# Kernel tuning notes

Measured on AMD Instinct MI355X. Metric: run time of the kernel, lower is better.

The kernel has to match this reference:

```python
import jax, jax.numpy as jnp
import numpy as np

EPS = 1e-5  # torch BatchNorm2d default


def _conv1x1(x, w):
    # x: [n, cin, h, w], w: [cout, cin] (1x1 conv == per-pixel matmul)
    return jnp.einsum('nchw,oc->nohw', x, w)


def _bn(x, gamma, beta, mean, var):
    # inference-mode BatchNorm2d over channel dim
    scale = gamma * jax.lax.rsqrt(var + EPS)
    shift = beta - mean * scale
    return x * scale[None, :, None, None] + shift[None, :, None, None]


def setup_inputs() -> dict:
    key = jax.random.key(0)
    ks = jax.random.split(key, 24)
    n, c, h, w = 16, 256, 64, 64
    width, planes = c // 2, c
    inp = {
        'x': jax.random.normal(ks[0], (n, c, h, w), jnp.float32),
        'w_theta': jax.random.normal(ks[1], (width, c), jnp.float32) * 0.05,
        'w_phi': jax.random.normal(ks[2], (width, c), jnp.float32) * 0.05,
        'w_g': jax.random.normal(ks[3], (width, c), jnp.float32) * 0.05,
        'w_zeta': jax.random.normal(ks[4], (planes, width), jnp.float32) * 0.05,
    }
    for i, (name, dim) in enumerate([('bn1', width), ('bn2', width), ('bn3', width), ('bn4', planes)]):
        k = 5 + 4 * i
        inp[f'{name}_gamma'] = jax.random.uniform(ks[k], (dim,), jnp.float32, 0.5, 1.5)
        inp[f'{name}_beta'] = jax.random.normal(ks[k + 1], (dim,), jnp.float32) * 0.1
        inp[f'{name}_mean'] = jax.random.normal(ks[k + 2], (dim,), jnp.float32) * 0.1
        inp[f'{name}_var'] = jax.random.uniform(ks[k + 3], (dim,), jnp.float32, 0.5, 1.5)
    return inp


def reference(x, w_theta, w_phi, w_g, w_zeta,
              bn1_gamma, bn1_beta, bn1_mean, bn1_var,
              bn2_gamma, bn2_beta, bn2_mean, bn2_var,
              bn3_gamma, bn3_beta, bn3_mean, bn3_var,
              bn4_gamma, bn4_beta, bn4_mean, bn4_var):
    n, c, h, w = x.shape
    theta = jax.nn.relu(_bn(_conv1x1(x, w_theta), bn1_gamma, bn1_beta, bn1_mean, bn1_var))
    phi = jax.nn.relu(_bn(_conv1x1(x, w_phi), bn2_gamma, bn2_beta, bn2_mean, bn2_var))
    g = jax.nn.relu(_bn(_conv1x1(x, w_g), bn3_gamma, bn3_beta, bn3_mean, bn3_var))

    width = theta.shape[1]
    hw = h * w
    theta = theta.reshape(n, width, hw)  # [n, C', S]
    phi = phi.reshape(n, width, hw)      # [n, C', S]
    g = g.reshape(n, width, hw)          # [n, C', S]

    # (theta^T @ phi) @ g^T == theta^T @ (phi @ g^T): no softmax, so associativity
    # lets us contract over pixels first -> O(S*C'^2) instead of O(S^2*C').
    kv = jnp.einsum('ncs,nds->ncd', phi, g)      # [n, C', C']
    out = jnp.einsum('ncs,ncd->nsd', theta, kv)  # [n, S, C']

    # faithful to torch: reshape (not transpose) [n, S, C'] -> [n, C', h, w]
    out = out.reshape(n, width, h, w)
    out = _bn(_conv1x1(out, w_zeta), bn4_gamma, bn4_beta, bn4_mean, bn4_var)
    return jax.nn.relu(out + x)
```

## Files before the change

kernel.cpp:

```cpp
#include <hip/hip_runtime.h>

#define BN_EPS 1e-5f

typedef unsigned short u16;
typedef __bf16 bf16x8 __attribute__((ext_vector_type(8)));
typedef float floatx4 __attribute__((ext_vector_type(4)));
typedef u16 u16x4 __attribute__((ext_vector_type(4)));
typedef u16 u16x8 __attribute__((ext_vector_type(8)));

__device__ __forceinline__ u16 f2bf(float f) {
    union { float f; unsigned int u; } v; v.f = f;
    unsigned int r = (v.u + 0x7fffu + ((v.u >> 16) & 1u)) >> 16;
    return (u16)r;
}

__device__ __forceinline__ unsigned int cvtpk(float lo, float hi) {
    unsigned int r;
    asm("v_cvt_pk_bf16_f32 %0, %1, %2" : "=v"(r) : "v"(lo), "v"(hi));
    return r;
}

__device__ __forceinline__ void gld16(const void* gsrc, void* ldst) {
    __builtin_amdgcn_global_load_lds(
        (const __attribute__((address_space(1))) unsigned int*)gsrc,
        (__attribute__((address_space(3))) unsigned int*)ldst, 16, 0, 0);
}

__device__ __forceinline__ int addsw(int seg, int s) {
    return (seg + (s & 7) + ((s >> 3) & 7)) & 7;
}

__global__ __launch_bounds__(256) void prep_kernel(
    const float* __restrict__ wt, const float* __restrict__ wp,
    const float* __restrict__ wg, const float* __restrict__ wz,
    const float* __restrict__ g1, const float* __restrict__ b1,
    const float* __restrict__ m1, const float* __restrict__ v1,
    const float* __restrict__ g2, const float* __restrict__ b2,
    const float* __restrict__ m2, const float* __restrict__ v2,
    const float* __restrict__ g3, const float* __restrict__ b3,
    const float* __restrict__ m3, const float* __restrict__ v3,
    const float* __restrict__ g4, const float* __restrict__ b4,
    const float* __restrict__ m4, const float* __restrict__ v4,
    u16* __restrict__ W1bf, float* __restrict__ shift1,
    u16* __restrict__ Wzbf, float* __restrict__ shift4)
{
    int id = blockIdx.x * 256 + threadIdx.x;
    if (id < 384 * 256) {
        int r = id >> 8, c = id & 255;
        int grp = r >> 7, ch = r & 127;
        const float* wsrc = grp == 0 ? wt : (grp == 1 ? wp : wg);
        const float* gg = grp == 0 ? g1 : (grp == 1 ? g2 : g3);
        const float* bb = grp == 0 ? b1 : (grp == 1 ? b2 : b3);
        const float* mm = grp == 0 ? m1 : (grp == 1 ? m2 : m3);
        const float* vv = grp == 0 ? v1 : (grp == 1 ? v2 : v3);
        float scale = gg[ch] * rsqrtf(vv[ch] + BN_EPS);
        W1bf[id] = f2bf(wsrc[ch * 256 + c] * scale);
        if (c == 0) shift1[r] = bb[ch] - mm[ch] * scale;
    }
    if (id < 256 * 128) {
        int o = id >> 7;
        float scale = g4[o] * rsqrtf(v4[o] + BN_EPS);
        Wzbf[id] = f2bf(wz[id] * scale);
        if ((id & 127) == 0) shift4[o] = b4[o] - m4[o] * scale;
    }
}

__global__ __launch_bounds__(512, 4) void gemm1_kernel(
    const float* __restrict__ x, const u16* __restrict__ W1,
    const float* __restrict__ shift1,
    u16* __restrict__ theta_sm, u16* __restrict__ pg)
{
    const int st = blockIdx.x, n = blockIdx.y;
    const int tid = threadIdx.x;
    const int w = tid >> 6, lane = tid & 63;
    const int quad = lane >> 4, l16 = lane & 15;

    __shared__ __align__(16) u16 ldsA[384 * 64];
    __shared__ __align__(16) u16 ldsB[64 * 64];

    floatx4 acc[3][4];
#pragma unroll
    for (int i = 0; i < 3; ++i)
#pragma unroll
        for (int j = 0; j < 4; ++j) acc[i][j] = floatx4{0.f, 0.f, 0.f, 0.f};

    const int s4 = tid & 15;
    const int cg = tid >> 4;
    const int slog = cg >> 2, dwin = cg & 3;
    const float* xb0 = x + ((size_t)n * 256 + 2 * cg) * 4096 + st * 64;
    unsigned int* ldsBdw = (unsigned int*)ldsB;

    float4 xv0 = *((const float4*)xb0 + s4);
    float4 xv1 = *((const float4*)(xb0 + 4096) + s4);

    for (int kc = 0; kc < 4; ++kc) {
        const float* f0 = (const float*)&xv0;
        const float* f1 = (const float*)&xv1;
#pragma unroll
        for (int j = 0; j < 4; ++j) {
            int s = 4 * s4 + j;
            ldsBdw[s * 32 + addsw(slog, s) * 4 + dwin] = cvtpk(f0[j], f1[j]);
        }
#pragma unroll
        for (int i = 0; i < 6; ++i) {
            int op = w * 6 + i;
            int r = op * 8 + (lane >> 3);
            int lseg = (lane & 7) ^ (r & 7);
            gld16(W1 + (size_t)r * 256 + kc * 64 + lseg * 8, ldsA + op * 512);
        }
        if (kc < 3) {
            xv0 = *((const float4*)(xb0 + (size_t)(kc + 1) * 64 * 4096) + s4);
            xv1 = *((const float4*)(xb0 + (size_t)((kc + 1) * 64 + 1) * 4096) + s4);
        }
        __syncthreads();

#pragma unroll
        for (int kk = 0; kk < 2; ++kk) {
            bf16x8 a[3];
#pragma unroll
            for (int mt = 0; mt < 3; ++mt) {
                int r = mt * 128 + w * 16 + l16;
                int phys = (kk * 4 + quad) ^ (r & 7);
                a[mt] = *(const bf16x8*)(ldsA + r * 64 + phys * 8);
            }
#pragma unroll
            for (int ni = 0; ni < 4; ++ni) {
                int s = ni * 16 + l16;
                int phys = addsw(kk * 4 + quad, s);
                bf16x8 b = *(const bf16x8*)(ldsB + s * 64 + phys * 8);
#pragma unroll
                for (int mt = 0; mt < 3; ++mt)
                    acc[mt][ni] = __builtin_amdgcn_mfma_f32_16x16x32_bf16(
                        a[mt], b, acc[mt][ni], 0, 0, 0);
            }
        }
        __syncthreads();
    }

    const int ocq = w * 16 + quad * 4;

    {
        float sh0 = shift1[ocq + 0], sh1 = shift1[ocq + 1];
        float sh2 = shift1[ocq + 2], sh3 = shift1[ocq + 3];
#pragma unroll
        for (int ni = 0; ni < 4; ++ni) {
            int s = st * 64 + ni * 16 + l16;
            float v0 = acc[0][ni][0] + sh0, v1 = acc[0][ni][1] + sh1;
            float v2 = acc[0][ni][2] + sh2, v3 = acc[0][ni][3] + sh3;
            v0 = v0 > 0.f ? v0 : 0.f;
            v1 = v1 > 0.f ? v1 : 0.f;
            v2 = v2 > 0.f ? v2 : 0.f;
            v3 = v3 > 0.f ? v3 : 0.f;
            uint2 pk;
            pk.x = cvtpk(v0, v1);
            pk.y = cvtpk(v2, v3);
            *(uint2*)(theta_sm + (size_t)n * 524288 + (size_t)s * 128 + ocq) = pk;
        }
    }

#pragma unroll
    for (int mt = 1; mt < 3; ++mt)
#pragma unroll
        for (int r = 0; r < 4; ++r) {
            int oc = mt * 128 + ocq + r;
            int prow = oc - 128;
            float sh = shift1[oc];
#pragma unroll
            for (int ni = 0; ni < 4; ++ni) {
                int s = st * 64 + ni * 16 + l16;
                float val = acc[mt][ni][r] + sh;
                val = val > 0.f ? val : 0.f;
                pg[(size_t)n * 1048576 + (size_t)prow * 4096 + s] = f2bf(val);
            }
        }
}

__global__ __launch_bounds__(512) void gemm2_kernel(
    const u16* __restrict__ pg, float* __restrict__ partials)
{
    const int kc = blockIdx.x, n = blockIdx.y;
    const int tid = threadIdx.x;
    const int w = tid >> 6, lane = tid & 63;
    const int quad = lane >> 4, l16 = lane & 15;

    __shared__ __align__(16) u16 ldsG[128 * 64];
    __shared__ __align__(16) u16 ldsP[128 * 64];

    floatx4 acc[2][4];
#pragma unroll
    for (int i = 0; i < 2; ++i)
#pragma unroll
        for (int j = 0; j < 4; ++j) acc[i][j] = floatx4{0.f, 0.f, 0.f, 0.f};

    const int d0 = (w >> 1) * 32, c0 = (w & 1) * 64;
    const u16* base = pg + (size_t)n * 1048576;

    for (int ch = 0; ch < 4; ++ch) {
        int s0 = kc * 256 + ch * 64;
#pragma unroll
        for (int i = 0; i < 2; ++i) {
            int op = w * 2 + i;
            int r = op * 8 + (lane >> 3);
            int lseg = (lane & 7) ^ (r & 7);
            gld16(base + (size_t)(128 + r) * 4096 + s0 + lseg * 8, ldsG + op * 512);
            gld16(base + (size_t)r * 4096 + s0 + lseg * 8, ldsP + op * 512);
        }
        __syncthreads();

#pragma unroll
        for (int kk = 0; kk < 2; ++kk) {
            bf16x8 a[2];
#pragma unroll
            for (int mi = 0; mi < 2; ++mi) {
                int r = d0 + mi * 16 + l16;
                int phys = (kk * 4 + quad) ^ (r & 7);
                a[mi] = *(const bf16x8*)(ldsG + r * 64 + phys * 8);
            }
#pragma unroll
            for (int ci = 0; ci < 4; ++ci) {
                int r = c0 + ci * 16 + l16;
                int phys = (kk * 4 + quad) ^ (r & 7);
                bf16x8 b = *(const bf16x8*)(ldsP + r * 64 + phys * 8);
#pragma unroll
                for (int mi = 0; mi < 2; ++mi)
                    acc[mi][ci] = __builtin_amdgcn_mfma_f32_16x16x32_bf16(
                        a[mi], b, acc[mi][ci], 0, 0, 0);
            }
        }
        __syncthreads();
    }

    float* outp = partials + (size_t)(n * 16 + kc) * 16384;
#pragma unroll
    for (int mi = 0; mi < 2; ++mi)
#pragma unroll
        for (int r = 0; r < 4; ++r) {
            int d = d0 + mi * 16 + quad * 4 + r;
#pragma unroll
            for (int ci = 0; ci < 4; ++ci)
                outp[d * 128 + c0 + ci * 16 + l16] = acc[mi][ci][r];
        }
}

__global__ __launch_bounds__(256) void kv_reduce_kernel(
    const float* __restrict__ partials, u16* __restrict__ kvT)
{
    int n = blockIdx.y;
    int f4 = blockIdx.x * 256 + threadIdx.x;
    const float4* p4 = (const float4*)partials;
    float4 s = {0.f, 0.f, 0.f, 0.f};
#pragma unroll
    for (int kc = 0; kc < 16; ++kc) {
        float4 v = p4[(size_t)(n * 16 + kc) * 4096 + f4];
        s.x += v.x; s.y += v.y; s.z += v.z; s.w += v.w;
    }
    u16x4 o; o[0] = f2bf(s.x); o[1] = f2bf(s.y); o[2] = f2bf(s.z); o[3] = f2bf(s.w);
    *(u16x4*)(kvT + (size_t)n * 16384 + f4 * 4) = o;
}

__global__ __launch_bounds__(256) void gemm3_kernel(
    const u16* __restrict__ theta_sm, const u16* __restrict__ kvT,
    u16* __restrict__ out_sd)
{
    const int st = blockIdx.x, n = blockIdx.y;
    const int tid = threadIdx.x;
    const int w = tid >> 6, lane = tid & 63;
    const int quad = lane >> 4, l16 = lane & 15;

    __shared__ __align__(16) u16 ldsT[128 * 64];
    __shared__ __align__(16) u16 ldsK[128 * 64];

    floatx4 acc[2][8];
#pragma unroll
    for (int i = 0; i < 2; ++i)
#pragma unroll
        for (int j = 0; j < 8; ++j) acc[i][j] = floatx4{0.f, 0.f, 0.f, 0.f};

    const u16* tbase = theta_sm + (size_t)n * 524288 + (size_t)st * 128 * 128;
    const u16* kbase = kvT + (size_t)n * 16384;

    for (int ch = 0; ch < 2; ++ch) {
#pragma unroll
        for (int i = 0; i < 4; ++i) {
            int op = w * 4 + i;
            int r = op * 8 + (lane >> 3);
            int lseg = (lane & 7) ^ (r & 7);
            gld16(tbase + (size_t)r * 128 + ch * 64 + lseg * 8, ldsT + op * 512);
            gld16(kbase + (size_t)r * 128 + ch * 64 + lseg * 8, ldsK + op * 512);
        }
        __syncthreads();

#pragma unroll
        for (int kk = 0; kk < 2; ++kk) {
            bf16x8 a[2];
#pragma unroll
            for (int mi = 0; mi < 2; ++mi) {
                int r = w * 32 + mi * 16 + l16;
                int phys = (kk * 4 + quad) ^ (r & 7);
                a[mi] = *(const bf16x8*)(ldsT + r * 64 + phys * 8);
            }
#pragma unroll
            for (int di = 0; di < 8; ++di) {
                int r = di * 16 + l16;
                int phys = (kk * 4 + quad) ^ (r & 7);
                bf16x8 b = *(const bf16x8*)(ldsK + r * 64 + phys * 8);
#pragma unroll
                for (int mi = 0; mi < 2; ++mi)
                    acc[mi][di] = __builtin_amdgcn_mfma_f32_16x16x32_bf16(
                        a[mi], b, acc[mi][di], 0, 0, 0);
            }
        }
        __syncthreads();
    }

#pragma unroll
    for (int mi = 0; mi < 2; ++mi)
#pragma unroll
        for (int r = 0; r < 4; ++r) {
            int s = st * 128 + w * 32 + mi * 16 + quad * 4 + r;
#pragma unroll
            for (int di = 0; di < 8; ++di)
                out_sd[(size_t)n * 524288 + (size_t)s * 128 + di * 16 + l16] =
                    f2bf(acc[mi][di][r]);
        }
}

__global__ __launch_bounds__(256) void gemm4_kernel(
    const u16* __restrict__ out_sd, const u16* __restrict__ Wz,
    const float* __restrict__ shift4, const float* __restrict__ x,
    float* __restrict__ out)
{
    const int st = blockIdx.x, ot = blockIdx.y, n = blockIdx.z;
    const int tid = threadIdx.x;
    const int w = tid >> 6, lane = tid & 63;
    const int quad = lane >> 4, l16 = lane & 15;

    __shared__ __align__(16) u16 ldsY[128 * 64];
    __shared__ __align__(16) u16 ldsW[128 * 64];

    floatx4 acc[2][8];
#pragma unroll
    for (int i = 0; i < 2; ++i)
#pragma unroll
        for (int j = 0; j < 8; ++j) acc[i][j] = floatx4{0.f, 0.f, 0.f, 0.f};

    const int sl = tid & 15;
    const int cg = tid >> 4;
    const u16* ybase = out_sd + (size_t)n * 524288 + st * 128;
    unsigned int* ldsYdw = (unsigned int*)ldsY;

    u16x8 yv0[2], yv1[2];
#pragma unroll
    for (int p = 0; p < 2; ++p) {
        int c0 = 2 * cg + 32 * p;
        yv0[p] = *(const u16x8*)(ybase + (size_t)c0 * 4096 + 8 * sl);
        yv1[p] = *(const u16x8*)(ybase + (size_t)(c0 + 1) * 4096 + 8 * sl);
    }

    for (int kc = 0; kc < 2; ++kc) {
#pragma unroll
        for (int p = 0; p < 2; ++p) {
            int cp = cg + 16 * p, slog = cp >> 2, dwin = cp & 3;
#pragma unroll
            for (int j = 0; j < 8; ++j) {
                int s = 8 * sl + j;
                unsigned int pk = (unsigned int)yv0[p][j] | ((unsigned int)yv1[p][j] << 16);
                ldsYdw[s * 32 + addsw(slog, s) * 4 + dwin] = pk;
            }
        }
#pragma unroll
        for (int i = 0; i < 4; ++i) {
            int op = w * 4 + i;
            int r = op * 8 + (lane >> 3);
            int lseg = (lane & 7) ^ (r & 7);
            gld16(Wz + (size_t)(ot * 128 + r) * 128 + kc * 64 + lseg * 8, ldsW + op * 512);
        }
        if (kc < 1) {
#pragma unroll
            for (int p = 0; p < 2; ++p) {
                int c0 = 2 * cg + 32 * p;
                yv0[p] = *(const u16x8*)(ybase + (size_t)(64 + c0) * 4096 + 8 * sl);
                yv1[p] = *(const u16x8*)(ybase + (size_t)(64 + c0 + 1) * 4096 + 8 * sl);
            }
        }
        __syncthreads();

#pragma unroll
        for (int kk = 0; kk < 2; ++kk) {
            bf16x8 a[2];
#pragma unroll
            for (int mi = 0; mi < 2; ++mi) {
                int r = w * 32 + mi * 16 + l16;
                int phys = (kk * 4 + quad) ^ (r & 7);
                a[mi] = *(const bf16x8*)(ldsW + r * 64 + phys * 8);
            }
#pragma unroll
            for (int ni = 0; ni < 8; ++ni) {
                int s = ni * 16 + l16;
                int phys = addsw(kk * 4 + quad, s);
                bf16x8 b = *(const bf16x8*)(ldsY + s * 64 + phys * 8);
#pragma unroll
                for (int mi = 0; mi < 2; ++mi)
                    acc[mi][ni] = __builtin_amdgcn_mfma_f32_16x16x32_bf16(
                        a[mi], b, acc[mi][ni], 0, 0, 0);
            }
        }
        __syncthreads();
    }

#pragma unroll
    for (int mi = 0; mi < 2; ++mi)
#pragma unroll
        for (int r = 0; r < 4; ++r) {
            int o = ot * 128 + w * 32 + mi * 16 + quad * 4 + r;
            float sh = shift4[o];
#pragma unroll
            for (int ni = 0; ni < 8; ++ni) {
                int s2 = st * 128 + ni * 16 + l16;
                size_t idx = ((size_t)n * 256 + o) * 4096 + s2;
                float val = acc[mi][ni][r] + sh + x[idx];
                out[idx] = val > 0.f ? val : 0.f;
            }
        }
}

extern "C" void kernel_launch(void* const* d_in, const int* in_sizes, int n_in,
                              void* d_out, int out_size, void* d_ws, size_t ws_size,
                              hipStream_t stream)
{
    const float* x  = (const float*)d_in[0];
    const float* wt = (const float*)d_in[1];
    const float* wp = (const float*)d_in[2];
    const float* wg = (const float*)d_in[3];
    const float* wz = (const float*)d_in[4];
    const float* bn[16];
    for (int i = 0; i < 16; ++i) bn[i] = (const float*)d_in[5 + i];

    char* ws = (char*)d_ws;
    u16*   W1bf     = (u16*)  (ws + 0);
    float* shift1   = (float*)(ws + 196608);
    u16*   Wzbf     = (u16*)  (ws + 198144);
    float* shift4   = (float*)(ws + 263680);
    u16*   theta_sm = (u16*)  (ws + 264704);
    u16*   pg       = (u16*)  (ws + 17041920);
    float* partials = (float*)(ws + 50596352);
    u16*   kvT      = (u16*)  (ws + 67373568);
    u16*   out_sd   = (u16*)  (ws + 67897856);
    float* out = (float*)d_out;

    prep_kernel<<<384, 256, 0, stream>>>(
        wt, wp, wg, wz,
        bn[0], bn[1], bn[2], bn[3],
        bn[4], bn[5], bn[6], bn[7],
        bn[8], bn[9], bn[10], bn[11],
        bn[12], bn[13], bn[14], bn[15],
        W1bf, shift1, Wzbf, shift4);

    gemm1_kernel<<<dim3(64, 16), 512, 0, stream>>>(x, W1bf, shift1, theta_sm, pg);
    gemm2_kernel<<<dim3(16, 16), 512, 0, stream>>>(pg, partials);
    kv_reduce_kernel<<<dim3(16, 16), 256, 0, stream>>>(partials, kvT);
    gemm3_kernel<<<dim3(32, 16), 256, 0, stream>>>(theta_sm, kvT, out_sd);
    gemm4_kernel<<<dim3(32, 2, 16), 256, 0, stream>>>(out_sd, Wzbf, shift4, x, out);
}
```

Baseline: 220.2 us.

## Double-buffer LDS in all GEMM kernels and widen gemm1 pixel tile

```diff
diff --git a/kernel.cpp b/kernel.cpp
--- a/kernel.cpp
+++ b/kernel.cpp
@@ -65,7 +65,7 @@
     }
 }
 
-__global__ __launch_bounds__(512, 4) void gemm1_kernel(
+__global__ __launch_bounds__(512, 2) void gemm1_kernel(
     const float* __restrict__ x, const u16* __restrict__ W1,
     const float* __restrict__ shift1,
     u16* __restrict__ theta_sm, u16* __restrict__ pg)
@@ -75,45 +75,48 @@
     const int w = tid >> 6, lane = tid & 63;
     const int quad = lane >> 4, l16 = lane & 15;
 
-    __shared__ __align__(16) u16 ldsA[384 * 64];
-    __shared__ __align__(16) u16 ldsB[64 * 64];
-
-    floatx4 acc[3][4];
+    __shared__ __align__(16) u16 ldsA[2][384 * 64];
+    __shared__ __align__(16) u16 ldsB[2][128 * 64];
+
+    floatx4 acc[3][8];
 #pragma unroll
     for (int i = 0; i < 3; ++i)
 #pragma unroll
-        for (int j = 0; j < 4; ++j) acc[i][j] = floatx4{0.f, 0.f, 0.f, 0.f};
-
-    const int s4 = tid & 15;
-    const int cg = tid >> 4;
-    const int slog = cg >> 2, dwin = cg & 3;
-    const float* xb0 = x + ((size_t)n * 256 + 2 * cg) * 4096 + st * 64;
-    unsigned int* ldsBdw = (unsigned int*)ldsB;
-
-    float4 xv0 = *((const float4*)xb0 + s4);
-    float4 xv1 = *((const float4*)(xb0 + 4096) + s4);
-
-    for (int kc = 0; kc < 4; ++kc) {
-        const float* f0 = (const float*)&xv0;
-        const float* f1 = (const float*)&xv1;
-#pragma unroll
-        for (int j = 0; j < 4; ++j) {
-            int s = 4 * s4 + j;
-            ldsBdw[s * 32 + addsw(slog, s) * 4 + dwin] = cvtpk(f0[j], f1[j]);
-        }
+        for (int j = 0; j < 8; ++j) acc[i][j] = floatx4{0.f, 0.f, 0.f, 0.f};
+
+    const int cp = w * 4 + quad;
+    const float* xb = x + ((size_t)n * 256 + 2 * cp) * 4096 + st * 128;
+
+    float4 xva[2][2], xvb[2][2];
+
+    auto loadx = [&](float4 (&xv)[2][2], int kc) {
+#pragma unroll
+        for (int ch = 0; ch < 2; ++ch)
+#pragma unroll
+            for (int hb = 0; hb < 2; ++hb)
+                xv[ch][hb] = *((const float4*)(xb + (size_t)(kc * 64 + ch) * 4096) + hb * 16 + l16);
+    };
+    auto writeB = [&](int buf, const float4 (&xv)[2][2]) {
+        unsigned int* bd = (unsigned int*)ldsB[buf];
+#pragma unroll
+        for (int hb = 0; hb < 2; ++hb)
+#pragma unroll
+            for (int j = 0; j < 4; ++j) {
+                int s = hb * 64 + l16 * 4 + j;
+                bd[s * 32 + addsw(w, s) * 4 + quad] =
+                    cvtpk(((const float*)&xv[0][hb])[j], ((const float*)&xv[1][hb])[j]);
+            }
+    };
+    auto stageA = [&](int buf, int kc) {
 #pragma unroll
         for (int i = 0; i < 6; ++i) {
             int op = w * 6 + i;
             int r = op * 8 + (lane >> 3);
             int lseg = (lane & 7) ^ (r & 7);
-            gld16(W1 + (size_t)r * 256 + kc * 64 + lseg * 8, ldsA + op * 512);
-        }
-        if (kc < 3) {
-            xv0 = *((const float4*)(xb0 + (size_t)(kc + 1) * 64 * 4096) + s4);
-            xv1 = *((const float4*)(xb0 + (size_t)((kc + 1) * 64 + 1) * 4096) + s4);
-        }
-        __syncthreads();
-
+            gld16(W1 + (size_t)r * 256 + kc * 64 + lseg * 8, ldsA[buf] + op * 512);
+        }
+    };
+    auto compute = [&](int buf) {
 #pragma unroll
         for (int kk = 0; kk < 2; ++kk) {
             bf16x8 a[3];
@@ -121,30 +124,50 @@
             for (int mt = 0; mt < 3; ++mt) {
                 int r = mt * 128 + w * 16 + l16;
                 int phys = (kk * 4 + quad) ^ (r & 7);
-                a[mt] = *(const bf16x8*)(ldsA + r * 64 + phys * 8);
-            }
-#pragma unroll
-            for (int ni = 0; ni < 4; ++ni) {
+                a[mt] = *(const bf16x8*)(ldsA[buf] + r * 64 + phys * 8);
+            }
+#pragma unroll
+            for (int ni = 0; ni < 8; ++ni) {
                 int s = ni * 16 + l16;
                 int phys = addsw(kk * 4 + quad, s);
-                bf16x8 b = *(const bf16x8*)(ldsB + s * 64 + phys * 8);
+                bf16x8 b = *(const bf16x8*)(ldsB[buf] + s * 64 + phys * 8);
 #pragma unroll
                 for (int mt = 0; mt < 3; ++mt)
                     acc[mt][ni] = __builtin_amdgcn_mfma_f32_16x16x32_bf16(
                         a[mt], b, acc[mt][ni], 0, 0, 0);
             }
         }
-        __syncthreads();
-    }
+    };
+
+    loadx(xva, 0);
+    stageA(0, 0);
+    writeB(0, xva);
+    loadx(xvb, 1);
+    __syncthreads();
+
+    loadx(xva, 2);
+    stageA(1, 1);
+    writeB(1, xvb);
+    compute(0);
+    __syncthreads();
+    loadx(xvb, 3);
+    stageA(0, 2);
+    writeB(0, xva);
+    compute(1);
+    __syncthreads();
+    stageA(1, 3);
+    writeB(1, xvb);
+    compute(0);
+    __syncthreads();
+    compute(1);
 
     const int ocq = w * 16 + quad * 4;
-
     {
         float sh0 = shift1[ocq + 0], sh1 = shift1[ocq + 1];
         float sh2 = shift1[ocq + 2], sh3 = shift1[ocq + 3];
 #pragma unroll
-        for (int ni = 0; ni < 4; ++ni) {
-            int s = st * 64 + ni * 16 + l16;
+        for (int ni = 0; ni < 8; ++ni) {
+            int s = st * 128 + ni * 16 + l16;
             float v0 = acc[0][ni][0] + sh0, v1 = acc[0][ni][1] + sh1;
             float v2 = acc[0][ni][2] + sh2, v3 = acc[0][ni][3] + sh3;
             v0 = v0 > 0.f ? v0 : 0.f;
@@ -157,7 +180,6 @@
             *(uint2*)(theta_sm + (size_t)n * 524288 + (size_t)s * 128 + ocq) = pk;
         }
     }
-
 #pragma unroll
     for (int mt = 1; mt < 3; ++mt)
 #pragma unroll
@@ -166,8 +188,8 @@
             int prow = oc - 128;
             float sh = shift1[oc];
 #pragma unroll
-            for (int ni = 0; ni < 4; ++ni) {
-                int s = st * 64 + ni * 16 + l16;
+            for (int ni = 0; ni < 8; ++ni) {
+                int s = st * 128 + ni * 16 + l16;
                 float val = acc[mt][ni][r] + sh;
                 val = val > 0.f ? val : 0.f;
                 pg[(size_t)n * 1048576 + (size_t)prow * 4096 + s] = f2bf(val);
@@ -183,8 +205,8 @@
     const int w = tid >> 6, lane = tid & 63;
     const int quad = lane >> 4, l16 = lane & 15;
 
-    __shared__ __align__(16) u16 ldsG[128 * 64];
-    __shared__ __align__(16) u16 ldsP[128 * 64];
+    __shared__ __align__(16) u16 ldsG[2][128 * 64];
+    __shared__ __align__(16) u16 ldsP[2][128 * 64];
 
     floatx4 acc[2][4];
 #pragma unroll
@@ -195,18 +217,18 @@
     const int d0 = (w >> 1) * 32, c0 = (w & 1) * 64;
     const u16* base = pg + (size_t)n * 1048576;
 
-    for (int ch = 0; ch < 4; ++ch) {
+    auto stage = [&](int buf, int ch) {
         int s0 = kc * 256 + ch * 64;
 #pragma unroll
         for (int i = 0; i < 2; ++i) {
             int op = w * 2 + i;
             int r = op * 8 + (lane >> 3);
             int lseg = (lane & 7) ^ (r & 7);
-            gld16(base + (size_t)(128 + r) * 4096 + s0 + lseg * 8, ldsG + op * 512);
-            gld16(base + (size_t)r * 4096 + s0 + lseg * 8, ldsP + op * 512);
-        }
-        __syncthreads();
-
+            gld16(base + (size_t)(128 + r) * 4096 + s0 + lseg * 8, ldsG[buf] + op * 512);
+            gld16(base + (size_t)r * 4096 + s0 + lseg * 8, ldsP[buf] + op * 512);
+        }
+    };
+    auto comp = [&](int buf) {
 #pragma unroll
         for (int kk = 0; kk < 2; ++kk) {
             bf16x8 a[2];
@@ -214,21 +236,26 @@
             for (int mi = 0; mi < 2; ++mi) {
                 int r = d0 + mi * 16 + l16;
                 int phys = (kk * 4 + quad) ^ (r & 7);
-                a[mi] = *(const bf16x8*)(ldsG + r * 64 + phys * 8);
+                a[mi] = *(const bf16x8*)(ldsG[buf] + r * 64 + phys * 8);
             }
 #pragma unroll
             for (int ci = 0; ci < 4; ++ci) {
                 int r = c0 + ci * 16 + l16;
                 int phys = (kk * 4 + quad) ^ (r & 7);
-                bf16x8 b = *(const bf16x8*)(ldsP + r * 64 + phys * 8);
+                bf16x8 b = *(const bf16x8*)(ldsP[buf] + r * 64 + phys * 8);
 #pragma unroll
                 for (int mi = 0; mi < 2; ++mi)
                     acc[mi][ci] = __builtin_amdgcn_mfma_f32_16x16x32_bf16(
                         a[mi], b, acc[mi][ci], 0, 0, 0);
             }
         }
-        __syncthreads();
-    }
+    };
+
+    stage(0, 0); __syncthreads();
+    stage(1, 1); comp(0); __syncthreads();
+    stage(0, 2); comp(1); __syncthreads();
+    stage(1, 3); comp(0); __syncthreads();
+    comp(1);
 
     float* outp = partials + (size_t)(n * 16 + kc) * 16384;
 #pragma unroll
@@ -267,8 +294,8 @@
     const int w = tid >> 6, lane = tid & 63;
     const int quad = lane >> 4, l16 = lane & 15;
 
-    __shared__ __align__(16) u16 ldsT[128 * 64];
-    __shared__ __align__(16) u16 ldsK[128 * 64];
+    __shared__ __align__(16) u16 ldsT[2][128 * 64];
+    __shared__ __align__(16) u16 ldsK[2][128 * 64];
 
     floatx4 acc[2][8];
 #pragma unroll
@@ -279,17 +306,17 @@
     const u16* tbase = theta_sm + (size_t)n * 524288 + (size_t)st * 128 * 128;
     const u16* kbase = kvT + (size_t)n * 16384;
 
-    for (int ch = 0; ch < 2; ++ch) {
+    auto stage = [&](int buf, int ch) {
 #pragma unroll
         for (int i = 0; i < 4; ++i) {
             int op = w * 4 + i;
             int r = op * 8 + (lane >> 3);
             int lseg = (lane & 7) ^ (r & 7);
-            gld16(tbase + (size_t)r * 128 + ch * 64 + lseg * 8, ldsT + op * 512);
-            gld16(kbase + (size_t)r * 128 + ch * 64 + lseg * 8, ldsK + op * 512);
-        }
-        __syncthreads();
-
+            gld16(tbase + (size_t)r * 128 + ch * 64 + lseg * 8, ldsT[buf] + op * 512);
+            gld16(kbase + (size_t)r * 128 + ch * 64 + lseg * 8, ldsK[buf] + op * 512);
+        }
+    };
+    auto comp = [&](int buf) {
 #pragma unroll
         for (int kk = 0; kk < 2; ++kk) {
             bf16x8 a[2];
@@ -297,21 +324,24 @@
             for (int mi = 0; mi < 2; ++mi) {
                 int r = w * 32 + mi * 16 + l16;
                 int phys = (kk * 4 + quad) ^ (r & 7);
-                a[mi] = *(const bf16x8*)(ldsT + r * 64 + phys * 8);
+                a[mi] = *(const bf16x8*)(ldsT[buf] + r * 64 + phys * 8);
             }
 #pragma unroll
             for (int di = 0; di < 8; ++di) {
                 int r = di * 16 + l16;
                 int phys = (kk * 4 + quad) ^ (r & 7);
-                bf16x8 b = *(const bf16x8*)(ldsK + r * 64 + phys * 8);
+                bf16x8 b = *(const bf16x8*)(ldsK[buf] + r * 64 + phys * 8);
 #pragma unroll
                 for (int mi = 0; mi < 2; ++mi)
                     acc[mi][di] = __builtin_amdgcn_mfma_f32_16x16x32_bf16(
                         a[mi], b, acc[mi][di], 0, 0, 0);
             }
         }
-        __syncthreads();
-    }
+    };
+
+    stage(0, 0); __syncthreads();
+    stage(1, 1); comp(0); __syncthreads();
+    comp(1);
 
 #pragma unroll
     for (int mi = 0; mi < 2; ++mi)
@@ -335,8 +365,8 @@
     const int w = tid >> 6, lane = tid & 63;
     const int quad = lane >> 4, l16 = lane & 15;
 
-    __shared__ __align__(16) u16 ldsY[128 * 64];
-    __shared__ __align__(16) u16 ldsW[128 * 64];
+    __shared__ __align__(16) u16 ldsY[2][128 * 64];
+    __shared__ __align__(16) u16 ldsW[2][128 * 64];
 
     floatx4 acc[2][8];
 #pragma unroll
@@ -347,44 +377,41 @@
     const int sl = tid & 15;
     const int cg = tid >> 4;
     const u16* ybase = out_sd + (size_t)n * 524288 + st * 128;
-    unsigned int* ldsYdw = (unsigned int*)ldsY;
-
-    u16x8 yv0[2], yv1[2];
-#pragma unroll
-    for (int p = 0; p < 2; ++p) {
-        int c0 = 2 * cg + 32 * p;
-        yv0[p] = *(const u16x8*)(ybase + (size_t)c0 * 4096 + 8 * sl);
-        yv1[p] = *(const u16x8*)(ybase + (size_t)(c0 + 1) * 4096 + 8 * sl);
-    }
-
-    for (int kc = 0; kc < 2; ++kc) {
+    unsigned int* ldsYdw0 = (unsigned int*)ldsY[0];
+    unsigned int* ldsYdw1 = (unsigned int*)ldsY[1];
+
+    u16x8 ya0[2], ya1[2], yb0[2], yb1[2];
+
+    auto loadY = [&](u16x8 (&y0)[2], u16x8 (&y1)[2], int kc) {
+#pragma unroll
+        for (int p = 0; p < 2; ++p) {
+            int c0 = 2 * cg + 32 * p + kc * 64;
+            y0[p] = *(const u16x8*)(ybase + (size_t)c0 * 4096 + 8 * sl);
+            y1[p] = *(const u16x8*)(ybase + (size_t)(c0 + 1) * 4096 + 8 * sl);
+        }
+    };
+    auto writeY = [&](unsigned int* yd, const u16x8 (&y0)[2], const u16x8 (&y1)[2]) {
 #pragma unroll
         for (int p = 0; p < 2; ++p) {
             int cp = cg + 16 * p, slog = cp >> 2, dwin = cp & 3;
 #pragma unroll
             for (int j = 0; j < 8; ++j) {
                 int s = 8 * sl + j;
-                unsigned int pk = (unsigned int)yv0[p][j] | ((unsigned int)yv1[p][j] << 16);
-                ldsYdw[s * 32 + addsw(slog, s) * 4 + dwin] = pk;
-            }
-        }
+                yd[s * 32 + addsw(slog, s) * 4 + dwin] =
+                    (unsigned int)y0[p][j] | ((unsigned int)y1[p][j] << 16);
+            }
+        }
+    };
+    auto stageW = [&](int buf, int kc) {
 #pragma unroll
         for (int i = 0; i < 4; ++i) {
             int op = w * 4 + i;
             int r = op * 8 + (lane >> 3);
             int lseg = (lane & 7) ^ (r & 7);
-            gld16(Wz + (size_t)(ot * 128 + r) * 128 + kc * 64 + lseg * 8, ldsW + op * 512);
-        }
-        if (kc < 1) {
-#pragma unroll
-            for (int p = 0; p < 2; ++p) {
-                int c0 = 2 * cg + 32 * p;
-                yv0[p] = *(const u16x8*)(ybase + (size_t)(64 + c0) * 4096 + 8 * sl);
-                yv1[p] = *(const u16x8*)(ybase + (size_t)(64 + c0 + 1) * 4096 + 8 * sl);
-            }
-        }
-        __syncthreads();
-
+            gld16(Wz + (size_t)(ot * 128 + r) * 128 + kc * 64 + lseg * 8, ldsW[buf] + op * 512);
+        }
+    };
+    auto comp = [&](int buf) {
 #pragma unroll
         for (int kk = 0; kk < 2; ++kk) {
             bf16x8 a[2];
@@ -392,21 +419,33 @@
             for (int mi = 0; mi < 2; ++mi) {
                 int r = w * 32 + mi * 16 + l16;
                 int phys = (kk * 4 + quad) ^ (r & 7);
-                a[mi] = *(const bf16x8*)(ldsW + r * 64 + phys * 8);
+                a[mi] = *(const bf16x8*)(ldsW[buf] + r * 64 + phys * 8);
             }
 #pragma unroll
             for (int ni = 0; ni < 8; ++ni) {
                 int s = ni * 16 + l16;
                 int phys = addsw(kk * 4 + quad, s);
-                bf16x8 b = *(const bf16x8*)(ldsY + s * 64 + phys * 8);
+                bf16x8 b = *(const bf16x8*)(ldsY[buf] + s * 64 + phys * 8);
 #pragma unroll
                 for (int mi = 0; mi < 2; ++mi)
                     acc[mi][ni] = __builtin_amdgcn_mfma_f32_16x16x32_bf16(
                         a[mi], b, acc[mi][ni], 0, 0, 0);
             }
         }
-        __syncthreads();
-    }
+    };
+
+    loadY(ya0, ya1, 0);
+    stageW(0, 0);
+    writeY(ldsYdw0, ya0, ya1);
+    loadY(yb0, yb1, 1);
+    __syncthreads();
+
+    stageW(1, 1);
+    writeY(ldsYdw1, yb0, yb1);
+    comp(0);
+    __syncthreads();
+
+    comp(1);
 
 #pragma unroll
     for (int mi = 0; mi < 2; ++mi)
@@ -456,7 +495,7 @@
         bn[12], bn[13], bn[14], bn[15],
         W1bf, shift1, Wzbf, shift4);
 
-    gemm1_kernel<<<dim3(64, 16), 512, 0, stream>>>(x, W1bf, shift1, theta_sm, pg);
+    gemm1_kernel<<<dim3(32, 16), 512, 0, stream>>>(x, W1bf, shift1, theta_sm, pg);
     gemm2_kernel<<<dim3(16, 16), 512, 0, stream>>>(pg, partials);
     kv_reduce_kernel<<<dim3(16, 16), 256, 0, stream>>>(partials, kvT);
     gemm3_kernel<<<dim3(32, 16), 256, 0, stream>>>(theta_sm, kvT, out_sd);
```

Measured after the change: 215.8 us. 1.02x faster.

## Fuse projection with KV accumulation and fuse output matmul with zeta conv

Applied to the files above, without the earlier changes.

```diff
diff --git a/kernel.cpp b/kernel.cpp
--- a/kernel.cpp
+++ b/kernel.cpp
@@ -65,181 +65,157 @@
     }
 }
 
-__global__ __launch_bounds__(512, 4) void gemm1_kernel(
+__global__ __launch_bounds__(512, 2) void k1_kernel(
     const float* __restrict__ x, const u16* __restrict__ W1,
     const float* __restrict__ shift1,
-    u16* __restrict__ theta_sm, u16* __restrict__ pg)
+    u16* __restrict__ theta_sm, float* __restrict__ partials)
 {
-    const int st = blockIdx.x, n = blockIdx.y;
+    const int sk = blockIdx.x, n = blockIdx.y;
     const int tid = threadIdx.x;
     const int w = tid >> 6, lane = tid & 63;
     const int quad = lane >> 4, l16 = lane & 15;
 
     __shared__ __align__(16) u16 ldsA[384 * 64];
-    __shared__ __align__(16) u16 ldsB[64 * 64];
-
-    floatx4 acc[3][4];
-#pragma unroll
-    for (int i = 0; i < 3; ++i)
-#pragma unroll
-        for (int j = 0; j < 4; ++j) acc[i][j] = floatx4{0.f, 0.f, 0.f, 0.f};
-
-    const int s4 = tid & 15;
-    const int cg = tid >> 4;
-    const int slog = cg >> 2, dwin = cg & 3;
-    const float* xb0 = x + ((size_t)n * 256 + 2 * cg) * 4096 + st * 64;
+    __shared__ __align__(16) u16 ldsB[128 * 64];
+    __shared__ __align__(16) u16 ldsPG[4][128 * 64];
+
+    floatx4 kv[8];
+#pragma unroll
+    for (int i = 0; i < 8; ++i) kv[i] = floatx4{0.f, 0.f, 0.f, 0.f};
+
+    const int cp = w * 4 + quad;
     unsigned int* ldsBdw = (unsigned int*)ldsB;
 
-    float4 xv0 = *((const float4*)xb0 + s4);
-    float4 xv1 = *((const float4*)(xb0 + 4096) + s4);
-
-    for (int kc = 0; kc < 4; ++kc) {
-        const float* f0 = (const float*)&xv0;
-        const float* f1 = (const float*)&xv1;
-#pragma unroll
-        for (int j = 0; j < 4; ++j) {
-            int s = 4 * s4 + j;
-            ldsBdw[s * 32 + addsw(slog, s) * 4 + dwin] = cvtpk(f0[j], f1[j]);
-        }
-#pragma unroll
-        for (int i = 0; i < 6; ++i) {
-            int op = w * 6 + i;
-            int r = op * 8 + (lane >> 3);
-            int lseg = (lane & 7) ^ (r & 7);
-            gld16(W1 + (size_t)r * 256 + kc * 64 + lseg * 8, ldsA + op * 512);
-        }
-        if (kc < 3) {
-            xv0 = *((const float4*)(xb0 + (size_t)(kc + 1) * 64 * 4096) + s4);
-            xv1 = *((const float4*)(xb0 + (size_t)((kc + 1) * 64 + 1) * 4096) + s4);
-        }
+    float4 xva[2][2], xvb[2][2];
+
+    for (int ss = 0; ss < 2; ++ss) {
+        const float* xb = x + ((size_t)n * 256 + 2 * cp) * 4096 + sk * 256 + ss * 128;
+
+        floatx4 acc[3][8];
+#pragma unroll
+        for (int i = 0; i < 3; ++i)
+#pragma unroll
+            for (int j = 0; j < 8; ++j) acc[i][j] = floatx4{0.f, 0.f, 0.f, 0.f};
+
+        auto loadx = [&](float4 (&xv)[2][2], int kc) {
+#pragma unroll
+            for (int ch = 0; ch < 2; ++ch)
+#pragma unroll
+                for (int hb = 0; hb < 2; ++hb)
+                    xv[ch][hb] = *((const float4*)(xb + (size_t)(kc * 64 + ch) * 4096) + hb * 16 + l16);
+        };
+        auto writeB = [&](const float4 (&xv)[2][2]) {
+#pragma unroll
+            for (int hb = 0; hb < 2; ++hb)
+#pragma unroll
+                for (int j = 0; j < 4; ++j) {
+                    int s = hb * 64 + l16 * 4 + j;
+                    ldsBdw[s * 32 + addsw(w, s) * 4 + quad] =
+                        cvtpk(((const float*)&xv[0][hb])[j], ((const float*)&xv[1][hb])[j]);
+                }
+        };
+        auto stageA = [&](int kc) {
+#pragma unroll
+            for (int i = 0; i < 6; ++i) {
+                int op = w * 6 + i;
+                int r = op * 8 + (lane >> 3);
+                int lseg = (lane & 7) ^ (r & 7);
+                gld16(W1 + (size_t)r * 256 + kc * 64 + lseg * 8, ldsA + op * 512);
+            }
+        };
+
+        loadx(xva, 0);
+        for (int kc = 0; kc < 4; ++kc) {
+            writeB((kc & 1) ? xvb : xva);
+            stageA(kc);
+            if (kc < 3) loadx((kc & 1) ? xva : xvb, kc + 1);
+            __syncthreads();
+#pragma unroll
+            for (int kk = 0; kk < 2; ++kk) {
+                bf16x8 a[3];
+#pragma unroll
+                for (int mt = 0; mt < 3; ++mt) {
+                    int r = mt * 128 + w * 16 + l16;
+                    int phys = (kk * 4 + quad) ^ (r & 7);
+                    a[mt] = *(const bf16x8*)(ldsA + r * 64 + phys * 8);
+                }
+#pragma unroll
+                for (int ni = 0; ni < 8; ++ni) {
+                    int s = ni * 16 + l16;
+                    int phys = addsw(kk * 4 + quad, s);
+                    bf16x8 b = *(const bf16x8*)(ldsB + s * 64 + phys * 8);
+#pragma unroll
+                    for (int mt = 0; mt < 3; ++mt)
+                        acc[mt][ni] = __builtin_amdgcn_mfma_f32_16x16x32_bf16(
+                            a[mt], b, acc[mt][ni], 0, 0, 0);
+                }
+            }
+            __syncthreads();
+        }
+
+        const int ocq = w * 16 + quad * 4;
+        {
+            float sh0 = shift1[ocq + 0], sh1 = shift1[ocq + 1];
+            float sh2 = shift1[ocq + 2], sh3 = shift1[ocq + 3];
+#pragma unroll
+            for (int ni = 0; ni < 8; ++ni) {
+                int s = sk * 256 + ss * 128 + ni * 16 + l16;
+                float v0 = acc[0][ni][0] + sh0, v1 = acc[0][ni][1] + sh1;
+                float v2 = acc[0][ni][2] + sh2, v3 = acc[0][ni][3] + sh3;
+                v0 = v0 > 0.f ? v0 : 0.f;
+                v1 = v1 > 0.f ? v1 : 0.f;
+                v2 = v2 > 0.f ? v2 : 0.f;
+                v3 = v3 > 0.f ? v3 : 0.f;
+                uint2 pk;
+                pk.x = cvtpk(v0, v1);
+                pk.y = cvtpk(v2, v3);
+                *(uint2*)(theta_sm + (size_t)n * 524288 + (size_t)s * 128 + ocq) = pk;
+            }
+        }
+#pragma unroll
+        for (int mt = 1; mt < 3; ++mt)
+#pragma unroll
+            for (int r = 0; r < 4; ++r) {
+                int ch = ocq + r;
+                float sh = shift1[mt * 128 + ch];
+#pragma unroll
+                for (int ni = 0; ni < 8; ++ni) {
+                    int sl = ni * 16 + l16;
+                    int half = sl >> 6, s6 = sl & 63;
+                    int phys = (s6 >> 3) ^ (ch & 7);
+                    float val = acc[mt][ni][r] + sh;
+                    val = val > 0.f ? val : 0.f;
+                    ldsPG[(mt - 1) * 2 + half][ch * 64 + phys * 8 + (s6 & 7)] = f2bf(val);
+                }
+            }
         __syncthreads();
 
 #pragma unroll
-        for (int kk = 0; kk < 2; ++kk) {
-            bf16x8 a[3];
-#pragma unroll
-            for (int mt = 0; mt < 3; ++mt) {
-                int r = mt * 128 + w * 16 + l16;
-                int phys = (kk * 4 + quad) ^ (r & 7);
-                a[mt] = *(const bf16x8*)(ldsA + r * 64 + phys * 8);
-            }
-#pragma unroll
-            for (int ni = 0; ni < 4; ++ni) {
-                int s = ni * 16 + l16;
-                int phys = addsw(kk * 4 + quad, s);
-                bf16x8 b = *(const bf16x8*)(ldsB + s * 64 + phys * 8);
-#pragma unroll
-                for (int mt = 0; mt < 3; ++mt)
-                    acc[mt][ni] = __builtin_amdgcn_mfma_f32_16x16x32_bf16(
-                        a[mt], b, acc[mt][ni], 0, 0, 0);
-            }
-        }
+        for (int h = 0; h < 2; ++h)
+#pragma unroll
+            for (int kk = 0; kk < 2; ++kk) {
+                int rd = w * 16 + l16;
+                int physa = (kk * 4 + quad) ^ (rd & 7);
+                bf16x8 a = *(const bf16x8*)(ldsPG[2 + h] + rd * 64 + physa * 8);
+#pragma unroll
+                for (int ci = 0; ci < 8; ++ci) {
+                    int rc = ci * 16 + l16;
+                    int physb = (kk * 4 + quad) ^ (rc & 7);
+                    bf16x8 b = *(const bf16x8*)(ldsPG[h] + rc * 64 + physb * 8);
+                    kv[ci] = __builtin_amdgcn_mfma_f32_16x16x32_bf16(a, b, kv[ci], 0, 0, 0);
+                }
+            }
         __syncthreads();
     }
 
-    const int ocq = w * 16 + quad * 4;
-
-    {
-        float sh0 = shift1[ocq + 0], sh1 = shift1[ocq + 1];
-        float sh2 = shift1[ocq + 2], sh3 = shift1[ocq + 3];
-#pragma unroll
-        for (int ni = 0; ni < 4; ++ni) {
-            int s = st * 64 + ni * 16 + l16;
-            float v0 = acc[0][ni][0] + sh0, v1 = acc[0][ni][1] + sh1;
-            float v2 = acc[0][ni][2] + sh2, v3 = acc[0][ni][3] + sh3;
-            v0 = v0 > 0.f ? v0 : 0.f;
-            v1 = v1 > 0.f ? v1 : 0.f;
-            v2 = v2 > 0.f ? v2 : 0.f;
-            v3 = v3 > 0.f ? v3 : 0.f;
-            uint2 pk;
-            pk.x = cvtpk(v0, v1);
-            pk.y = cvtpk(v2, v3);
-            *(uint2*)(theta_sm + (size_t)n * 524288 + (size_t)s * 128 + ocq) = pk;
-        }
-    }
-
-#pragma unroll
-    for (int mt = 1; mt < 3; ++mt)
-#pragma unroll
-        for (int r = 0; r < 4; ++r) {
-            int oc = mt * 128 + ocq + r;
-            int prow = oc - 128;
-            float sh = shift1[oc];
-#pragma unroll
-            for (int ni = 0; ni < 4; ++ni) {
-                int s = st * 64 + ni * 16 + l16;
-                float val = acc[mt][ni][r] + sh;
-                val = val > 0.f ? val : 0.f;
-                pg[(size_t)n * 1048576 + (size_t)prow * 4096 + s] = f2bf(val);
-            }
-        }
-}
-
-__global__ __launch_bounds__(512) void gemm2_kernel(
-    const u16* __restrict__ pg, float* __restrict__ partials)
-{
-    const int kc = blockIdx.x, n = blockIdx.y;
-    const int tid = threadIdx.x;
-    const int w = tid >> 6, lane = tid & 63;
-    const int quad = lane >> 4, l16 = lane & 15;
-
-    __shared__ __align__(16) u16 ldsG[128 * 64];
-    __shared__ __align__(16) u16 ldsP[128 * 64];
-
-    floatx4 acc[2][4];
-#pragma unroll
-    for (int i = 0; i < 2; ++i)
-#pragma unroll
-        for (int j = 0; j < 4; ++j) acc[i][j] = floatx4{0.f, 0.f, 0.f, 0.f};
-
-    const int d0 = (w >> 1) * 32, c0 = (w & 1) * 64;
-    const u16* base = pg + (size_t)n * 1048576;
-
-    for (int ch = 0; ch < 4; ++ch) {
-        int s0 = kc * 256 + ch * 64;
-#pragma unroll
-        for (int i = 0; i < 2; ++i) {
-            int op = w * 2 + i;
-            int r = op * 8 + (lane >> 3);
-            int lseg = (lane & 7) ^ (r & 7);
-            gld16(base + (size_t)(128 + r) * 4096 + s0 + lseg * 8, ldsG + op * 512);
-            gld16(base + (size_t)r * 4096 + s0 + lseg * 8, ldsP + op * 512);
-        }
-        __syncthreads();
-
-#pragma unroll
-        for (int kk = 0; kk < 2; ++kk) {
-            bf16x8 a[2];
-#pragma unroll
-            for (int mi = 0; mi < 2; ++mi) {
-                int r = d0 + mi * 16 + l16;
-                int phys = (kk * 4 + quad) ^ (r & 7);
-                a[mi] = *(const bf16x8*)(ldsG + r * 64 + phys * 8);
-            }
-#pragma unroll
-            for (int ci = 0; ci < 4; ++ci) {
-                int r = c0 + ci * 16 + l16;
-                int phys = (kk * 4 + quad) ^ (r & 7);
-                bf16x8 b = *(const bf16x8*)(ldsP + r * 64 + phys * 8);
-#pragma unroll
-                for (int mi = 0; mi < 2; ++mi)
-                    acc[mi][ci] = __builtin_amdgcn_mfma_f32_16x16x32_bf16(
-                        a[mi], b, acc[mi][ci], 0, 0, 0);
-            }
-        }
-        __syncthreads();
-    }
-
-    float* outp = partials + (size_t)(n * 16 + kc) * 16384;
-#pragma unroll
-    for (int mi = 0; mi < 2; ++mi)
-#pragma unroll
-        for (int r = 0; r < 4; ++r) {
-            int d = d0 + mi * 16 + quad * 4 + r;
-#pragma unroll
-            for (int ci = 0; ci < 4; ++ci)
-                outp[d * 128 + c0 + ci * 16 + l16] = acc[mi][ci][r];
-        }
+    float* outp = partials + (size_t)(n * 16 + sk) * 16384;
+#pragma unroll
+    for (int r = 0; r < 4; ++r) {
+        int d = w * 16 + quad * 4 + r;
+#pragma unroll
+        for (int ci = 0; ci < 8; ++ci)
+            outp[d * 128 + ci * 16 + l16] = kv[ci][r];
+    }
 }
 
 __global__ __launch_bounds__(256) void kv_reduce_kernel(
@@ -258,38 +234,90 @@
     *(u16x4*)(kvT + (size_t)n * 16384 + f4 * 4) = o;
 }
 
-__global__ __launch_bounds__(256) void gemm3_kernel(
+__global__ __launch_bounds__(512, 2) void k34_kernel(
     const u16* __restrict__ theta_sm, const u16* __restrict__ kvT,
-    u16* __restrict__ out_sd)
+    const u16* __restrict__ Wz, const float* __restrict__ shift4,
+    const float* __restrict__ x, float* __restrict__ out)
 {
     const int st = blockIdx.x, n = blockIdx.y;
     const int tid = threadIdx.x;
     const int w = tid >> 6, lane = tid & 63;
     const int quad = lane >> 4, l16 = lane & 15;
 
-    __shared__ __align__(16) u16 ldsT[128 * 64];
-    __shared__ __align__(16) u16 ldsK[128 * 64];
-
-    floatx4 acc[2][8];
-#pragma unroll
-    for (int i = 0; i < 2; ++i)
-#pragma unroll
-        for (int j = 0; j < 8; ++j) acc[i][j] = floatx4{0.f, 0.f, 0.f, 0.f};
-
-    const u16* tbase = theta_sm + (size_t)n * 524288 + (size_t)st * 128 * 128;
+    __shared__ __align__(16) u16 lds[49152];
+    u16* T0 = lds;
+    u16* K0 = lds + 8192;
+    u16* T1 = lds + 16384;
+    u16* K1 = lds + 24576;
+    u16* Y  = lds + 32768;
+
+    const u16* tbase = theta_sm + (size_t)n * 524288 + (size_t)st * 128;
     const u16* kbase = kvT + (size_t)n * 16384;
 
-    for (int ch = 0; ch < 2; ++ch) {
-#pragma unroll
-        for (int i = 0; i < 4; ++i) {
-            int op = w * 4 + i;
+    floatx4 acc3[8];
+#pragma unroll
+    for (int i = 0; i < 8; ++i) acc3[i] = floatx4{0.f, 0.f, 0.f, 0.f};
+
+    auto stageTK = [&](u16* T, u16* K, int ch) {
+#pragma unroll
+        for (int i = 0; i < 2; ++i) {
+            int op = w * 2 + i;
             int r = op * 8 + (lane >> 3);
             int lseg = (lane & 7) ^ (r & 7);
-            gld16(tbase + (size_t)r * 128 + ch * 64 + lseg * 8, ldsT + op * 512);
-            gld16(kbase + (size_t)r * 128 + ch * 64 + lseg * 8, ldsK + op * 512);
-        }
-        __syncthreads();
-
+            gld16(tbase + (size_t)r * 4096 + ch * 64 + lseg * 8, T + op * 512);
+            gld16(kbase + (size_t)r * 128 + ch * 64 + lseg * 8, K + op * 512);
+        }
+    };
+    auto comp3 = [&](const u16* T, const u16* K) {
+#pragma unroll
+        for (int kk = 0; kk < 2; ++kk) {
+            int rc2 = w * 16 + l16;
+            int physa = (kk * 4 + quad) ^ (rc2 & 7);
+            bf16x8 a = *(const bf16x8*)(T + rc2 * 64 + physa * 8);
+#pragma unroll
+            for (int di = 0; di < 8; ++di) {
+                int rd = di * 16 + l16;
+                int physb = (kk * 4 + quad) ^ (rd & 7);
+                bf16x8 b = *(const bf16x8*)(K + rd * 64 + physb * 8);
+                acc3[di] = __builtin_amdgcn_mfma_f32_16x16x32_bf16(a, b, acc3[di], 0, 0, 0);
+            }
+        }
+    };
+
+    stageTK(T0, K0, 0);
+    __syncthreads();
+    stageTK(T1, K1, 1);
+    comp3(T0, K0);
+    __syncthreads();
+    comp3(T1, K1);
+
+#pragma unroll
+    for (int di = 0; di < 8; ++di) {
+        int j = di * 16 + l16;
+#pragma unroll
+        for (int r = 0; r < 4; ++r) {
+            int c2 = w * 16 + quad * 4 + r;
+            int half = c2 >> 6, c64 = c2 & 63;
+            int phys = (c64 >> 3) ^ (j & 7);
+            Y[half * 8192 + j * 64 + phys * 8 + (c64 & 7)] = f2bf(acc3[di][r]);
+        }
+    }
+#pragma unroll
+    for (int i = 0; i < 4; ++i) {
+        int op = w * 4 + i;
+        int r = op * 8 + (lane >> 3);
+        int lseg = (lane & 7) ^ (r & 7);
+        gld16(Wz + (size_t)r * 128 + 0 * 64 + lseg * 8, lds + op * 512);
+    }
+    __syncthreads();
+
+    floatx4 acc4[2][8];
+#pragma unroll
+    for (int i = 0; i < 2; ++i)
+#pragma unroll
+        for (int j = 0; j < 8; ++j) acc4[i][j] = floatx4{0.f, 0.f, 0.f, 0.f};
+
+    auto comp4 = [&](const u16* WL, int ch) {
 #pragma unroll
         for (int kk = 0; kk < 2; ++kk) {
             bf16x8 a[2];
@@ -297,128 +325,43 @@
             for (int mi = 0; mi < 2; ++mi) {
                 int r = w * 32 + mi * 16 + l16;
                 int phys = (kk * 4 + quad) ^ (r & 7);
-                a[mi] = *(const bf16x8*)(ldsT + r * 64 + phys * 8);
-            }
-#pragma unroll
-            for (int di = 0; di < 8; ++di) {
-                int r = di * 16 + l16;
-                int phys = (kk * 4 + quad) ^ (r & 7);
-                bf16x8 b = *(const bf16x8*)(ldsK + r * 64 + phys * 8);
-#pragma unroll
-                for (int mi = 0; mi < 2; ++mi)
-                    acc[mi][di] = __builtin_amdgcn_mfma_f32_16x16x32_bf16(
-                        a[mi], b, acc[mi][di], 0, 0, 0);
-            }
-        }
-        __syncthreads();
-    }
-
-#pragma unroll
-    for (int mi = 0; mi < 2; ++mi)
-#pragma unroll
-        for (int r = 0; r < 4; ++r) {
-            int s = st * 128 + w * 32 + mi * 16 + quad * 4 + r;
-#pragma unroll
-            for (int di = 0; di < 8; ++di)
-                out_sd[(size_t)n * 524288 + (size_t)s * 128 + di * 16 + l16] =
-                    f2bf(acc[mi][di][r]);
-        }
-}
-
-__global__ __launch_bounds__(256) void gemm4_kernel(
-    const u16* __restrict__ out_sd, const u16* __restrict__ Wz,
-    const float* __restrict__ shift4, const float* __restrict__ x,
-    float* __restrict__ out)
-{
-    const int st = blockIdx.x, ot = blockIdx.y, n = blockIdx.z;
-    const int tid = threadIdx.x;
-    const int w = tid >> 6, lane = tid & 63;
-    const int quad = lane >> 4, l16 = lane & 15;
-
-    __shared__ __align__(16) u16 ldsY[128 * 64];
-    __shared__ __align__(16) u16 ldsW[128 * 64];
-
-    floatx4 acc[2][8];
-#pragma unroll
-    for (int i = 0; i < 2; ++i)
-#pragma unroll
-        for (int j = 0; j < 8; ++j) acc[i][j] = floatx4{0.f, 0.f, 0.f, 0.f};
-
-    const int sl = tid & 15;
-    const int cg = tid >> 4;
-    const u16* ybase = out_sd + (size_t)n * 524288 + st * 128;
-    unsigned int* ldsYdw = (unsigned int*)ldsY;
-
-    u16x8 yv0[2], yv1[2];
-#pragma unroll
-    for (int p = 0; p < 2; ++p) {
-        int c0 = 2 * cg + 32 * p;
-        yv0[p] = *(const u16x8*)(ybase + (size_t)c0 * 4096 + 8 * sl);
-        yv1[p] = *(const u16x8*)(ybase + (size_t)(c0 + 1) * 4096 + 8 * sl);
-    }
-
-    for (int kc = 0; kc < 2; ++kc) {
-#pragma unroll
-        for (int p = 0; p < 2; ++p) {
-            int cp = cg + 16 * p, slog = cp >> 2, dwin = cp & 3;
-#pragma unroll
-            for (int j = 0; j < 8; ++j) {
-                int s = 8 * sl + j;
-                unsigned int pk = (unsigned int)yv0[p][j] | ((unsigned int)yv1[p][j] << 16);
-                ldsYdw[s * 32 + addsw(slog, s) * 4 + dwin] = pk;
-            }
-        }
-#pragma unroll
-        for (int i = 0; i < 4; ++i) {
-            int op = w * 4 + i;
-            int r = op * 8 + (lane >> 3);
-            int lseg = (lane & 7) ^ (r & 7);
-            gld16(Wz + (size_t)(ot * 128 + r) * 128 + kc * 64 + lseg * 8, ldsW + op * 512);
-        }
-        if (kc < 1) {
-#pragma unroll
-            for (int p = 0; p < 2; ++p) {
-                int c0 = 2 * cg + 32 * p;
-                yv0[p] = *(const u16x8*)(ybase + (size_t)(64 + c0) * 4096 + 8 * sl);
-                yv1[p] = *(const u16x8*)(ybase + (size_t)(64 + c0 + 1) * 4096 + 8 * sl);
-            }
-        }
-        __syncthreads();
-
-#pragma unroll
-        for (int kk = 0; kk < 2; ++kk) {
-            bf16x8 a[2];
-#pragma unroll
-            for (int mi = 0; mi < 2; ++mi) {
-                int r = w * 32 + mi * 16 + l16;
-                int phys = (kk * 4 + quad) ^ (r & 7);
-                a[mi] = *(const bf16x8*)(ldsW + r * 64 + phys * 8);
+                a[mi] = *(const bf16x8*)(WL + r * 64 + phys * 8);
             }
 #pragma unroll
             for (int ni = 0; ni < 8; ++ni) {
                 int s = ni * 16 + l16;
-                int phys = addsw(kk * 4 + quad, s);
-                bf16x8 b = *(const bf16x8*)(ldsY + s * 64 + phys * 8);
+                int phys = (kk * 4 + quad) ^ (s & 7);
+                bf16x8 b = *(const bf16x8*)(Y + ch * 8192 + s * 64 + phys * 8);
 #pragma unroll
                 for (int mi = 0; mi < 2; ++mi)
-                    acc[mi][ni] = __builtin_amdgcn_mfma_f32_16x16x32_bf16(
-                        a[mi], b, acc[mi][ni], 0, 0, 0);
-            }
-        }
-        __syncthreads();
-    }
+                    acc4[mi][ni] = __builtin_amdgcn_mfma_f32_16x16x32_bf16(
+                        a[mi], b, acc4[mi][ni], 0, 0, 0);
+            }
+        }
+    };
+
+#pragma unroll
+    for (int i = 0; i < 4; ++i) {
+        int op = w * 4 + i;
+        int r = op * 8 + (lane >> 3);
+        int lseg = (lane & 7) ^ (r & 7);
+        gld16(Wz + (size_t)r * 128 + 1 * 64 + lseg * 8, lds + 16384 + op * 512);
+    }
+    comp4(lds, 0);
+    __syncthreads();
+    comp4(lds + 16384, 1);
 
 #pragma unroll
     for (int mi = 0; mi < 2; ++mi)
 #pragma unroll
         for (int r = 0; r < 4; ++r) {
-            int o = ot * 128 + w * 32 + mi * 16 + quad * 4 + r;
+            int o = w * 32 + mi * 16 + quad * 4 + r;
             float sh = shift4[o];
 #pragma unroll
             for (int ni = 0; ni < 8; ++ni) {
                 int s2 = st * 128 + ni * 16 + l16;
                 size_t idx = ((size_t)n * 256 + o) * 4096 + s2;
-                float val = acc[mi][ni][r] + sh + x[idx];
+                float val = acc4[mi][ni][r] + sh + x[idx];
                 out[idx] = val > 0.f ? val : 0.f;
             }
         }
@@ -442,10 +385,8 @@
     u16*   Wzbf     = (u16*)  (ws + 198144);
     float* shift4   = (float*)(ws + 263680);
     u16*   theta_sm = (u16*)  (ws + 264704);
-    u16*   pg       = (u16*)  (ws + 17041920);
-    float* partials = (float*)(ws + 50596352);
-    u16*   kvT      = (u16*)  (ws + 67373568);
-    u16*   out_sd   = (u16*)  (ws + 67897856);
+    float* partials = (float*)(ws + 17041920);
+    u16*   kvT      = (u16*)  (ws + 33819136);
     float* out = (float*)d_out;
 
     prep_kernel<<<384, 256, 0, stream>>>(
@@ -456,9 +397,7 @@
         bn[12], bn[13], bn[14], bn[15],
         W1bf, shift1, Wzbf, shift4);
 
-    gemm1_kernel<<<dim3(64, 16), 512, 0, stream>>>(x, W1bf, shift1, theta_sm, pg);
-    gemm2_kernel<<<dim3(16, 16), 512, 0, stream>>>(pg, partials);
+    k1_kernel<<<dim3(16, 16), 512, 0, stream>>>(x, W1bf, shift1, theta_sm, partials);
     kv_reduce_kernel<<<dim3(16, 16), 256, 0, stream>>>(partials, kvT);
-    gemm3_kernel<<<dim3(32, 16), 256, 0, stream>>>(theta_sm, kvT, out_sd);
-    gemm4_kernel<<<dim3(32, 2, 16), 256, 0, stream>>>(out_sd, Wzbf, shift4, x, out);
-}
+    k34_kernel<<<dim3(32, 16), 512, 0, stream>>>(theta_sm, kvT, Wzbf, shift4, x, out);
+}
```

Result: no change. 221.6 us (+0.7%).
